# Optimization experiments

Hardware: AMD Instinct MI355X
Metric: run time of the kernel (lower is better)

The kernel has to match this reference:

```python
import jax, jax.numpy as jnp
import numpy as np

H = 16
D_MODEL = 1024
D_K = D_MODEL // H
WINDOW = 50
ROPE_BASE = 10000.0


def _rope_tables(seq_len, dim, dtype):
    inv_freq = 1.0 / (ROPE_BASE ** (jnp.arange(0, dim, 2, dtype=jnp.float32) / dim))
    t = jnp.arange(seq_len, dtype=jnp.float32)
    freqs = t[:, None] * inv_freq[None, :]          # [S, dim/2]
    emb = jnp.concatenate([freqs, freqs], axis=-1)  # [S, dim]
    return jnp.cos(emb).astype(dtype), jnp.sin(emb).astype(dtype)


def _rotate_half(x):
    d = x.shape[-1] // 2
    return jnp.concatenate([-x[..., d:], x[..., :d]], axis=-1)


def setup_inputs() -> dict:
    key = jax.random.key(0)
    ks = jax.random.split(key, 11)
    B, S = 2, 2048
    scale = 1.0 / np.sqrt(D_MODEL)
    inp = {
        'query': jax.random.normal(ks[0], (B, S, D_MODEL), jnp.float32),
        'key':   jax.random.normal(ks[1], (B, S, D_MODEL), jnp.float32),
        'value': jax.random.normal(ks[2], (B, S, D_MODEL), jnp.float32),
        'Wq': jax.random.normal(ks[3], (D_MODEL, D_MODEL), jnp.float32) * scale,
        'bq': jnp.zeros((D_MODEL,), jnp.float32),
        'Wk': jax.random.normal(ks[4], (D_MODEL, D_MODEL), jnp.float32) * scale,
        'bk': jnp.zeros((D_MODEL,), jnp.float32),
        'Wv': jax.random.normal(ks[5], (D_MODEL, D_MODEL), jnp.float32) * scale,
        'bv': jnp.zeros((D_MODEL,), jnp.float32),
        'Wo': jax.random.normal(ks[6], (D_MODEL, D_MODEL), jnp.float32) * scale,
        'bo': jnp.zeros((D_MODEL,), jnp.float32),
    }
    return inp


def reference(query, key, value, Wq, bq, Wk, bk, Wv, bv, Wo, bo):
    B, S, _ = query.shape
    # QKV projections (torch Linear: x @ W.T + b), split into heads -> [B,H,S,Dk]
    def proj(x, W, b):
        return (x @ W.T + b).reshape(B, S, H, D_K).transpose(0, 2, 1, 3)
    q = proj(query, Wq, bq)
    k = proj(key, Wk, bk)
    v = proj(value, Wv, bv)

    cos, sin = _rope_tables(S, D_K, q.dtype)  # [S, Dk]
    q = q * cos + _rotate_half(q) * sin
    k = k * cos + _rotate_half(k) * sin

    scores = jnp.einsum('bhqd,bhkd->bhqk', q, k) / np.sqrt(D_K)
    # sliding-window mask: |i-j| <= WINDOW
    idx = jnp.arange(S)
    dist = jnp.abs(idx[None, :] - idx[:, None])  # [S, S]
    scores = jnp.where(dist <= WINDOW, scores, jnp.asarray(-1e9, scores.dtype))

    p = jax.nn.softmax(scores, axis=-1)
    out = jnp.einsum('bhqk,bhkd->bhqd', p, v)          # [B,H,S,Dk]
    out = out.transpose(0, 2, 1, 3).reshape(B, S, D_MODEL)
    return out @ Wo.T + bo
```

## Files before the change

kernel.cpp:

```cpp
#include <hip/hip_runtime.h>
#include <hip/hip_bf16.h>
#include <math.h>

typedef __bf16 bf16_t;
typedef __bf16 bf16x8 __attribute__((ext_vector_type(8)));
typedef float floatx4 __attribute__((ext_vector_type(4)));
typedef unsigned int u32;

#define NHEAD 16

__device__ __forceinline__ void gload_lds16(const void* g, void* l) {
    __builtin_amdgcn_global_load_lds((const __attribute__((address_space(1))) u32*)g,
                                     (__attribute__((address_space(3))) u32*)l, 16, 0, 0);
}

__global__ __launch_bounds__(256) void k_prep(
    const float* __restrict__ q, const float* __restrict__ k, const float* __restrict__ v,
    const float* __restrict__ wq, const float* __restrict__ wk,
    const float* __restrict__ wv, const float* __restrict__ wo,
    bf16_t* __restrict__ Xq, bf16_t* __restrict__ Xk, bf16_t* __restrict__ Xv,
    bf16_t* __restrict__ Wqb, bf16_t* __restrict__ Wkb, bf16_t* __restrict__ Wvb,
    bf16_t* __restrict__ Wob, float* __restrict__ ct, float* __restrict__ st)
{
    int b = blockIdx.x;
    if (b < 8192) {
        const float* src; bf16_t* dst; int off;
        if      (b < 2048) { src = q;  dst = Xq;  off = b; }
        else if (b < 4096) { src = k;  dst = Xk;  off = b - 2048; }
        else if (b < 6144) { src = v;  dst = Xv;  off = b - 4096; }
        else if (b < 6656) { src = wq; dst = Wqb; off = b - 6144; }
        else if (b < 7168) { src = wk; dst = Wkb; off = b - 6656; }
        else if (b < 7680) { src = wv; dst = Wvb; off = b - 7168; }
        else               { src = wo; dst = Wob; off = b - 7680; }
        int i = (off * 256 + threadIdx.x) * 8;
        float4 a = *(const float4*)(src + i);
        float4 c = *(const float4*)(src + i + 4);
        bf16x8 o;
        o[0]=(bf16_t)a.x; o[1]=(bf16_t)a.y; o[2]=(bf16_t)a.z; o[3]=(bf16_t)a.w;
        o[4]=(bf16_t)c.x; o[5]=(bf16_t)c.y; o[6]=(bf16_t)c.z; o[7]=(bf16_t)c.w;
        *(bf16x8*)(dst + i) = o;
    } else {
        int idx = (b - 8192) * 256 + threadIdx.x;
        int s = idx >> 5, i = idx & 31;
        float e = (float)(2 * i) / 64.0f;
        float invf = 1.0f / powf(10000.0f, e);
        float ang = (float)s * invf;
        ct[idx] = cosf(ang);
        st[idx] = sinf(ang);
    }
}

__global__ __launch_bounds__(256,5) void k_gemm_qkv(
    const bf16_t* __restrict__ Xq, const bf16_t* __restrict__ Xk, const bf16_t* __restrict__ Xv,
    const bf16_t* __restrict__ Wqb, const bf16_t* __restrict__ Wkb, const bf16_t* __restrict__ Wvb,
    const float* __restrict__ bq, const float* __restrict__ bk, const float* __restrict__ bv,
    bf16_t* __restrict__ Qr, bf16_t* __restrict__ Kr, bf16_t* __restrict__ Vh,
    const float* __restrict__ ct, const float* __restrict__ st)
{
    __shared__ __align__(16) bf16_t As[2][4096];
    __shared__ __align__(16) bf16_t Bs[2][2048];

    int b0 = blockIdx.x;
    int wg = (b0 & 7) * 192 + (b0 >> 3);
    int id  = wg >> 9;
    int bid = wg & 511;
    int bmt = bid >> 4, bnt = bid & 15;

    const bf16_t* A   = (id==0) ? Xq  : (id==1) ? Xk  : Xv;
    const bf16_t* Wt  = (id==0) ? Wqb : (id==1) ? Wkb : Wvb;
    const float*  bias= (id==0) ? bq  : (id==1) ? bk  : bv;
    bf16_t* out = (id==0) ? Qr : (id==1) ? Kr : Vh;
    bool do_rope = (id < 2);

    int bm = bmt << 7;
    int bn = bnt << 6;
    int tid = threadIdx.x;
    int l = tid & 63, wid = tid >> 6;
    int fr = l & 15, kg = l >> 4;

    floatx4 acc[2][4];
    #pragma unroll
    for (int i = 0; i < 2; ++i)
        #pragma unroll
        for (int j = 0; j < 4; ++j) acc[i][j] = (floatx4){0.f,0.f,0.f,0.f};

    int srow = tid >> 2, scol = (tid & 3) << 3;
    const bf16_t* Ap0 = A  + ((size_t)(bm + srow) << 10) + scol;
    const bf16_t* Ap1 = A  + ((size_t)(bm + 64 + srow) << 10) + scol;
    const bf16_t* Bp  = Wt + ((size_t)(bn + srow) << 10) + scol;

    gload_lds16(Ap0, &As[0][tid << 3]);
    gload_lds16(Ap1, &As[0][(tid + 256) << 3]);
    gload_lds16(Bp,  &Bs[0][tid << 3]);
    __syncthreads();

    int cur = 0;
    for (int t = 0; t < 32; ++t) {
        if (t < 31) {
            int k0 = (t + 1) << 5;
            gload_lds16(Ap0 + k0, &As[cur ^ 1][tid << 3]);
            gload_lds16(Ap1 + k0, &As[cur ^ 1][(tid + 256) << 3]);
            gload_lds16(Bp  + k0, &Bs[cur ^ 1][tid << 3]);
        }
        bf16x8 af[2], bfr[4];
        #pragma unroll
        for (int i = 0; i < 2; ++i)
            af[i]  = *(const bf16x8*)&As[cur][((wid << 5) + (i << 4) + fr) * 32 + (kg << 3)];
        #pragma unroll
        for (int j = 0; j < 4; ++j)
            bfr[j] = *(const bf16x8*)&Bs[cur][((j << 4) + fr) * 32 + (kg << 3)];
        #pragma unroll
        for (int i = 0; i < 2; ++i)
            #pragma unroll
            for (int j = 0; j < 4; ++j)
                acc[i][j] = __builtin_amdgcn_mfma_f32_16x16x32_bf16(af[i], bfr[j], acc[i][j], 0, 0, 0);
        __syncthreads();
        cur ^= 1;
    }

    int h = bnt;
    #pragma unroll
    for (int i = 0; i < 2; ++i) {
        #pragma unroll
        for (int r = 0; r < 4; ++r) {
            int m  = bm + (wid << 5) + (i << 4) + (kg << 2) + r;
            int b_ = m >> 11, s_ = m & 2047;
            size_t ob = ((((size_t)(b_ * NHEAD + h)) << 11) + s_) << 6;
            if (do_rope) {
                #pragma unroll
                for (int j = 0; j < 2; ++j) {
                    int d = (j << 4) + fr;
                    float lo = acc[i][j][r]     + bias[bn + d];
                    float hv = acc[i][j + 2][r] + bias[bn + d + 32];
                    float c = ct[(s_ << 5) + d], sn = st[(s_ << 5) + d];
                    out[ob + d]      = (bf16_t)(lo * c - hv * sn);
                    out[ob + d + 32] = (bf16_t)(hv * c + lo * sn);
                }
            } else {
                #pragma unroll
                for (int j = 0; j < 4; ++j) {
                    int d = (j << 4) + fr;
                    out[ob + d] = (bf16_t)(acc[i][j][r] + bias[bn + d]);
                }
            }
        }
    }
}

__global__ __launch_bounds__(256,4) void k_gemm_o(
    const bf16_t* __restrict__ A, const bf16_t* __restrict__ Wt,
    const float* __restrict__ bias, float* __restrict__ out)
{
    __shared__ __align__(16) bf16_t As[2][2048];
    __shared__ __align__(16) bf16_t Bs[2][2048];

    int b0 = blockIdx.x;
    int wg = (b0 & 7) * 128 + (b0 >> 3);
    int bm = (wg >> 4) << 6;
    int bn = (wg & 15) << 6;
    int tid = threadIdx.x;
    int l = tid & 63, wid = tid >> 6;
    int fr = l & 15, kg = l >> 4;

    floatx4 acc[4];
    #pragma unroll
    for (int j = 0; j < 4; ++j) acc[j] = (floatx4){0.f,0.f,0.f,0.f};

    int srow = tid >> 2, scol = (tid & 3) << 3;
    const bf16_t* Ap = A  + ((size_t)(bm + srow) << 10) + scol;
    const bf16_t* Bp = Wt + ((size_t)(bn + srow) << 10) + scol;

    gload_lds16(Ap, &As[0][tid << 3]);
    gload_lds16(Bp, &Bs[0][tid << 3]);
    __syncthreads();

    int cur = 0;
    for (int t = 0; t < 32; ++t) {
        if (t < 31) {
            int k0 = (t + 1) << 5;
            gload_lds16(Ap + k0, &As[cur ^ 1][tid << 3]);
            gload_lds16(Bp + k0, &Bs[cur ^ 1][tid << 3]);
        }
        bf16x8 af, bfr[4];
        af = *(const bf16x8*)&As[cur][((wid << 4) + fr) * 32 + (kg << 3)];
        #pragma unroll
        for (int j = 0; j < 4; ++j)
            bfr[j] = *(const bf16x8*)&Bs[cur][((j << 4) + fr) * 32 + (kg << 3)];
        #pragma unroll
        for (int j = 0; j < 4; ++j)
            acc[j] = __builtin_amdgcn_mfma_f32_16x16x32_bf16(af, bfr[j], acc[j], 0, 0, 0);
        __syncthreads();
        cur ^= 1;
    }

    #pragma unroll
    for (int r = 0; r < 4; ++r) {
        int m = bm + (wid << 4) + (kg << 2) + r;
        #pragma unroll
        for (int j = 0; j < 4; ++j) {
            int n = bn + (j << 4) + fr;
            out[((size_t)m << 10) + n] = acc[j][r] + bias[n];
        }
    }
}

__global__ __launch_bounds__(256,2) void k_attn(
    const bf16_t* __restrict__ Qr, const bf16_t* __restrict__ Kr,
    const bf16_t* __restrict__ Vh, bf16_t* __restrict__ AO)
{
    __shared__ char smem[51200];
    bf16_t* KsPs = (bf16_t*)smem;
    bf16_t* Vt   = (bf16_t*)(smem + 25600);

    int q0 = blockIdx.x << 6;
    int h = blockIdx.y, b_ = blockIdx.z;
    int kstart = q0 - 64; if (kstart < 0) kstart = 0;
    int kend   = q0 + 128; if (kend > 2048) kend = 2048;
    int NR = kend - kstart;

    int tid = threadIdx.x, l = tid & 63, w = tid >> 6;
    int lane16 = l & 15, hi8 = (l >> 4) << 3;

    const bf16_t* Kbase = Kr + (((((size_t)(b_*NHEAD + h)) << 11) + kstart) << 6);
    const bf16_t* Vbase = Vh + (((((size_t)(b_*NHEAD + h)) << 11) + kstart) << 6);

    #pragma unroll
    for (int it = 0; it < 6; ++it) {
        int c = tid + (it << 8);
        int y = c << 4;
        int row = y >> 7, oz = y & 127;
        int srw = row < NR ? row : NR - 1;
        int src = (srw << 7) + (oz ^ ((row & 7) << 4));
        gload_lds16((const char*)Kbase + src, (char*)KsPs + y);
    }
    #pragma unroll
    for (int it = 0; it < 6; ++it) {
        int c = tid + (it << 8);
        int jd = c >> 3, d0 = (c & 7) << 3;
        int js = jd < NR ? jd : NR - 1;
        bf16x8 v8 = *(const bf16x8*)(Vbase + (js << 6) + d0);
        #pragma unroll
        for (int t = 0; t < 8; ++t) Vt[(d0 + t) * 200 + jd] = v8[t];
    }
    int qs = q0 + (w << 4) + lane16;
    const bf16_t* Qbase = Qr + (((((size_t)(b_*NHEAD + h)) << 11) + qs) << 6);
    bf16x8 qf0 = *(const bf16x8*)(Qbase + hi8);
    bf16x8 qf1 = *(const bf16x8*)(Qbase + 32 + hi8);

    __syncthreads();

    floatx4 sc[12];
    #pragma unroll
    for (int kt = 0; kt < 12; ++kt) {
        int row = (kt << 4) + lane16;
        int base = (row << 7) + (hi8 << 1);
        int swz = (row & 7) << 4;
        bf16x8 kf0 = *(const bf16x8*)((const char*)KsPs + (base ^ swz));
        bf16x8 kf1 = *(const bf16x8*)((const char*)KsPs + ((base + 64) ^ swz));
        floatx4 a = (floatx4){0.f,0.f,0.f,0.f};
        a = __builtin_amdgcn_mfma_f32_16x16x32_bf16(qf0, kf0, a, 0, 0, 0);
        a = __builtin_amdgcn_mfma_f32_16x16x32_bf16(qf1, kf1, a, 0, 0, 0);
        sc[kt] = a;
    }

    float inv_[4];
    #pragma unroll
    for (int r = 0; r < 4; ++r) {
        int qrow = q0 + (w << 4) + ((l >> 4) << 2) + r;
        float mx = -1e30f;
        #pragma unroll
        for (int kt = 0; kt < 12; ++kt) {
            int ks = kstart + (kt << 4) + lane16;
            int dd = qrow - ks; dd = dd < 0 ? -dd : dd;
            float sv = sc[kt][r] * 0.125f;
            sv = (dd <= 50 && ks < kend) ? sv : -1e30f;
            sc[kt][r] = sv;
            mx = fmaxf(mx, sv);
        }
        #pragma unroll
        for (int off = 1; off < 16; off <<= 1) mx = fmaxf(mx, __shfl_xor(mx, off));
        float sum = 0.f;
        #pragma unroll
        for (int kt = 0; kt < 12; ++kt) {
            float p = __expf(sc[kt][r] - mx);
            sc[kt][r] = p;
            sum += p;
        }
        #pragma unroll
        for (int off = 1; off < 16; off <<= 1) sum += __shfl_xor(sum, off);
        inv_[r] = 1.0f / sum;
    }

    __syncthreads();

    bf16_t* Pw = KsPs + w * 16 * 200;
    #pragma unroll
    for (int r = 0; r < 4; ++r) {
        int prow = ((l >> 4) << 2) + r;
        #pragma unroll
        for (int kt = 0; kt < 12; ++kt)
            Pw[prow * 200 + (kt << 4) + lane16] = (bf16_t)(sc[kt][r] * inv_[r]);
    }

    floatx4 oc[4];
    #pragma unroll
    for (int dt = 0; dt < 4; ++dt) oc[dt] = (floatx4){0.f,0.f,0.f,0.f};
    #pragma unroll
    for (int ks = 0; ks < 6; ++ks) {
        bf16x8 pf = *(const bf16x8*)&Pw[lane16 * 200 + (ks << 5) + hi8];
        #pragma unroll
        for (int dt = 0; dt < 4; ++dt) {
            bf16x8 vf = *(const bf16x8*)&Vt[((dt << 4) + lane16) * 200 + (ks << 5) + hi8];
            oc[dt] = __builtin_amdgcn_mfma_f32_16x16x32_bf16(pf, vf, oc[dt], 0, 0, 0);
        }
    }
    #pragma unroll
    for (int dt = 0; dt < 4; ++dt)
        #pragma unroll
        for (int r = 0; r < 4; ++r) {
            int qq = q0 + (w << 4) + ((l >> 4) << 2) + r;
            AO[(((size_t)(b_ * 2048 + qq)) << 10) + (h << 6) + (dt << 4) + lane16] = (bf16_t)oc[dt][r];
        }
}

extern "C" void kernel_launch(void* const* d_in, const int* in_sizes, int n_in,
                              void* d_out, int out_size, void* d_ws, size_t ws_size,
                              hipStream_t stream)
{
    const float* query = (const float*)d_in[0];
    const float* key_  = (const float*)d_in[1];
    const float* value = (const float*)d_in[2];
    const float* Wq = (const float*)d_in[3];
    const float* bq = (const float*)d_in[4];
    const float* Wk = (const float*)d_in[5];
    const float* bk = (const float*)d_in[6];
    const float* Wv = (const float*)d_in[7];
    const float* bv = (const float*)d_in[8];
    const float* Wo = (const float*)d_in[9];
    const float* bo = (const float*)d_in[10];

    char* ws = (char*)d_ws;
    bf16_t* Xq  = (bf16_t*)(ws);
    bf16_t* Xk  = (bf16_t*)(ws + 8388608);
    bf16_t* Xv  = (bf16_t*)(ws + 16777216);
    bf16_t* Wqb = (bf16_t*)(ws + 25165824);
    bf16_t* Wkb = (bf16_t*)(ws + 27262976);
    bf16_t* Wvb = (bf16_t*)(ws + 29360128);
    bf16_t* Wob = (bf16_t*)(ws + 31457280);
    bf16_t* Qr  = (bf16_t*)(ws + 33554432);
    bf16_t* Kr  = (bf16_t*)(ws + 41943040);
    bf16_t* Vh  = (bf16_t*)(ws + 50331648);
    bf16_t* AO  = (bf16_t*)(ws + 58720256);
    float*  ct  = (float*)(ws + 67108864);
    float*  st  = (float*)(ws + 67371008);

    k_prep<<<8448, 256, 0, stream>>>(query, key_, value, Wq, Wk, Wv, Wo,
                                     Xq, Xk, Xv, Wqb, Wkb, Wvb, Wob, ct, st);
    k_gemm_qkv<<<1536, 256, 0, stream>>>(Xq, Xk, Xv, Wqb, Wkb, Wvb,
                                         bq, bk, bv, Qr, Kr, Vh, ct, st);
    k_attn<<<dim3(32, 16, 2), 256, 0, stream>>>(Qr, Kr, Vh, AO);
    k_gemm_o<<<1024, 256, 0, stream>>>(AO, Wob, bo, (float*)d_out);
}
```

Baseline: 104.1 us.

## Enlarge QKV GEMM tiles to 128x128 and swizzle LDS layouts

The QKV projection GEMM moves from 128x64 to 128x128 block tiles on a 2x2 wave grid, halving the grid and raising operand reuse per LDS load. Both GEMMs reorder their global-to-LDS staging so each 16-row MFMA fragment sits in a contiguous 1KB chunk, aimed at avoiding LDS bank conflicts on fragment reads. The attention kernel adds XOR swizzles to the transposed V and P buffers for the same reason, and its occupancy hint rises from 2 to 3. The larger tile needs more accumulator registers and LDS per block, which lowers occupancy for the QKV GEMM.

```diff
diff --git a/kernel.cpp b/kernel.cpp
--- a/kernel.cpp
+++ b/kernel.cpp
@@ -50,7 +50,8 @@
     }
 }
 
-__global__ __launch_bounds__(256,5) void k_gemm_qkv(
+
+__global__ __launch_bounds__(256,3) void k_gemm_qkv(
     const bf16_t* __restrict__ Xq, const bf16_t* __restrict__ Xk, const bf16_t* __restrict__ Xv,
     const bf16_t* __restrict__ Wqb, const bf16_t* __restrict__ Wkb, const bf16_t* __restrict__ Wvb,
     const float* __restrict__ bq, const float* __restrict__ bk, const float* __restrict__ bv,
@@ -58,13 +59,12 @@
     const float* __restrict__ ct, const float* __restrict__ st)
 {
     __shared__ __align__(16) bf16_t As[2][4096];
-    __shared__ __align__(16) bf16_t Bs[2][2048];
+    __shared__ __align__(16) bf16_t Bs[2][4096];
 
     int b0 = blockIdx.x;
-    int wg = (b0 & 7) * 192 + (b0 >> 3);
-    int id  = wg >> 9;
-    int bid = wg & 511;
-    int bmt = bid >> 4, bnt = bid & 15;
+    int wg = (b0 & 7) * 96 + (b0 >> 3);
+    int id  = wg >> 8;
+    int bid = wg & 255;
 
     const bf16_t* A   = (id==0) ? Xq  : (id==1) ? Xk  : Xv;
     const bf16_t* Wt  = (id==0) ? Wqb : (id==1) ? Wkb : Wvb;
@@ -72,45 +72,50 @@
     bf16_t* out = (id==0) ? Qr : (id==1) ? Kr : Vh;
     bool do_rope = (id < 2);
 
-    int bm = bmt << 7;
-    int bn = bnt << 6;
+    int bm = (bid >> 3) << 7;
+    int bn = (bid & 7) << 7;
     int tid = threadIdx.x;
     int l = tid & 63, wid = tid >> 6;
+    int wr = wid >> 1, wc = wid & 1;
     int fr = l & 15, kg = l >> 4;
 
-    floatx4 acc[2][4];
-    #pragma unroll
-    for (int i = 0; i < 2; ++i)
+    floatx4 acc[4][4];
+    #pragma unroll
+    for (int i = 0; i < 4; ++i)
         #pragma unroll
         for (int j = 0; j < 4; ++j) acc[i][j] = (floatx4){0.f,0.f,0.f,0.f};
 
-    int srow = tid >> 2, scol = (tid & 3) << 3;
-    const bf16_t* Ap0 = A  + ((size_t)(bm + srow) << 10) + scol;
-    const bf16_t* Ap1 = A  + ((size_t)(bm + 64 + srow) << 10) + scol;
-    const bf16_t* Bp  = Wt + ((size_t)(bn + srow) << 10) + scol;
-
-    gload_lds16(Ap0, &As[0][tid << 3]);
-    gload_lds16(Ap1, &As[0][(tid + 256) << 3]);
-    gload_lds16(Bp,  &Bs[0][tid << 3]);
+    int c0 = tid, c1 = tid + 256;
+    int row0 = ((c0 >> 6) << 4) + (c0 & 15), sl0 = ((c0 >> 4) & 3) << 3;
+    int row1 = ((c1 >> 6) << 4) + (c1 & 15), sl1 = ((c1 >> 4) & 3) << 3;
+    const bf16_t* Ap0 = A  + ((size_t)(bm + row0) << 10) + sl0;
+    const bf16_t* Ap1 = A  + ((size_t)(bm + row1) << 10) + sl1;
+    const bf16_t* Bp0 = Wt + ((size_t)(bn + row0) << 10) + sl0;
+    const bf16_t* Bp1 = Wt + ((size_t)(bn + row1) << 10) + sl1;
+
+    gload_lds16(Ap0, &As[0][c0 << 3]);  gload_lds16(Ap1, &As[0][c1 << 3]);
+    gload_lds16(Bp0, &Bs[0][c0 << 3]);  gload_lds16(Bp1, &Bs[0][c1 << 3]);
     __syncthreads();
 
+    int a_off = (kg << 8) + (fr << 4);
     int cur = 0;
     for (int t = 0; t < 32; ++t) {
         if (t < 31) {
             int k0 = (t + 1) << 5;
-            gload_lds16(Ap0 + k0, &As[cur ^ 1][tid << 3]);
-            gload_lds16(Ap1 + k0, &As[cur ^ 1][(tid + 256) << 3]);
-            gload_lds16(Bp  + k0, &Bs[cur ^ 1][tid << 3]);
-        }
-        bf16x8 af[2], bfr[4];
-        #pragma unroll
-        for (int i = 0; i < 2; ++i)
-            af[i]  = *(const bf16x8*)&As[cur][((wid << 5) + (i << 4) + fr) * 32 + (kg << 3)];
+            gload_lds16(Ap0 + k0, &As[cur ^ 1][c0 << 3]);
+            gload_lds16(Ap1 + k0, &As[cur ^ 1][c1 << 3]);
+            gload_lds16(Bp0 + k0, &Bs[cur ^ 1][c0 << 3]);
+            gload_lds16(Bp1 + k0, &Bs[cur ^ 1][c1 << 3]);
+        }
+        bf16x8 af[4], bfr[4];
+        #pragma unroll
+        for (int i = 0; i < 4; ++i)
+            af[i]  = *(const bf16x8*)((const char*)As[cur] + (((wr << 2) + i) << 10) + a_off);
         #pragma unroll
         for (int j = 0; j < 4; ++j)
-            bfr[j] = *(const bf16x8*)&Bs[cur][((j << 4) + fr) * 32 + (kg << 3)];
-        #pragma unroll
-        for (int i = 0; i < 2; ++i)
+            bfr[j] = *(const bf16x8*)((const char*)Bs[cur] + (((wc << 2) + j) << 10) + a_off);
+        #pragma unroll
+        for (int i = 0; i < 4; ++i)
             #pragma unroll
             for (int j = 0; j < 4; ++j)
                 acc[i][j] = __builtin_amdgcn_mfma_f32_16x16x32_bf16(af[i], bfr[j], acc[i][j], 0, 0, 0);
@@ -118,29 +123,29 @@
         cur ^= 1;
     }
 
-    int h = bnt;
-    #pragma unroll
-    for (int i = 0; i < 2; ++i) {
+    int h = (bn + (wc<<6)) >> 6;
+    #pragma unroll
+    for (int i = 0; i < 4; ++i) {
         #pragma unroll
         for (int r = 0; r < 4; ++r) {
-            int m  = bm + (wid << 5) + (i << 4) + (kg << 2) + r;
+            int m  = bm + (wr<<6) + (i<<4) + (kg<<2) + r;
             int b_ = m >> 11, s_ = m & 2047;
-            size_t ob = ((((size_t)(b_ * NHEAD + h)) << 11) + s_) << 6;
+            size_t ob = ((((size_t)(b_*NHEAD + h)) << 11) + s_) << 6;
             if (do_rope) {
                 #pragma unroll
                 for (int j = 0; j < 2; ++j) {
-                    int d = (j << 4) + fr;
-                    float lo = acc[i][j][r]     + bias[bn + d];
-                    float hv = acc[i][j + 2][r] + bias[bn + d + 32];
-                    float c = ct[(s_ << 5) + d], sn = st[(s_ << 5) + d];
-                    out[ob + d]      = (bf16_t)(lo * c - hv * sn);
-                    out[ob + d + 32] = (bf16_t)(hv * c + lo * sn);
+                    int d = (j<<4) + fr;
+                    float lo = acc[i][j][r]   + bias[bn + (wc<<6) + d];
+                    float hv = acc[i][j+2][r] + bias[bn + (wc<<6) + d + 32];
+                    float c = ct[(s_<<5) + d], sn = st[(s_<<5) + d];
+                    out[ob + d]      = (bf16_t)(lo*c - hv*sn);
+                    out[ob + d + 32] = (bf16_t)(hv*c + lo*sn);
                 }
             } else {
                 #pragma unroll
                 for (int j = 0; j < 4; ++j) {
-                    int d = (j << 4) + fr;
-                    out[ob + d] = (bf16_t)(acc[i][j][r] + bias[bn + d]);
+                    int d = (j<<4) + fr;
+                    out[ob + d] = (bf16_t)(acc[i][j][r] + bias[bn + (wc<<6) + d]);
                 }
             }
         }
@@ -166,14 +171,15 @@
     #pragma unroll
     for (int j = 0; j < 4; ++j) acc[j] = (floatx4){0.f,0.f,0.f,0.f};
 
-    int srow = tid >> 2, scol = (tid & 3) << 3;
-    const bf16_t* Ap = A  + ((size_t)(bm + srow) << 10) + scol;
-    const bf16_t* Bp = Wt + ((size_t)(bn + srow) << 10) + scol;
+    int row0 = ((tid >> 6) << 4) + (tid & 15), sl0 = ((tid >> 4) & 3) << 3;
+    const bf16_t* Ap = A  + ((size_t)(bm + row0) << 10) + sl0;
+    const bf16_t* Bp = Wt + ((size_t)(bn + row0) << 10) + sl0;
 
     gload_lds16(Ap, &As[0][tid << 3]);
     gload_lds16(Bp, &Bs[0][tid << 3]);
     __syncthreads();
 
+    int a_off = (kg << 8) + (fr << 4);
     int cur = 0;
     for (int t = 0; t < 32; ++t) {
         if (t < 31) {
@@ -182,10 +188,10 @@
             gload_lds16(Bp + k0, &Bs[cur ^ 1][tid << 3]);
         }
         bf16x8 af, bfr[4];
-        af = *(const bf16x8*)&As[cur][((wid << 4) + fr) * 32 + (kg << 3)];
+        af = *(const bf16x8*)((const char*)As[cur] + (wid << 10) + a_off);
         #pragma unroll
         for (int j = 0; j < 4; ++j)
-            bfr[j] = *(const bf16x8*)&Bs[cur][((j << 4) + fr) * 32 + (kg << 3)];
+            bfr[j] = *(const bf16x8*)((const char*)Bs[cur] + (j << 10) + a_off);
         #pragma unroll
         for (int j = 0; j < 4; ++j)
             acc[j] = __builtin_amdgcn_mfma_f32_16x16x32_bf16(af, bfr[j], acc[j], 0, 0, 0);
@@ -204,13 +210,13 @@
     }
 }
 
-__global__ __launch_bounds__(256,2) void k_attn(
+__global__ __launch_bounds__(256,3) void k_attn(
     const bf16_t* __restrict__ Qr, const bf16_t* __restrict__ Kr,
     const bf16_t* __restrict__ Vh, bf16_t* __restrict__ AO)
 {
     __shared__ char smem[51200];
-    bf16_t* KsPs = (bf16_t*)smem;
-    bf16_t* Vt   = (bf16_t*)(smem + 25600);
+    char* KsPs = smem;
+    char* VtB  = smem + 25600;
 
     int q0 = blockIdx.x << 6;
     int h = blockIdx.y, b_ = blockIdx.z;
@@ -231,7 +237,7 @@
         int row = y >> 7, oz = y & 127;
         int srw = row < NR ? row : NR - 1;
         int src = (srw << 7) + (oz ^ ((row & 7) << 4));
-        gload_lds16((const char*)Kbase + src, (char*)KsPs + y);
+        gload_lds16((const char*)Kbase + src, KsPs + y);
     }
     #pragma unroll
     for (int it = 0; it < 6; ++it) {
@@ -240,7 +246,11 @@
         int js = jd < NR ? jd : NR - 1;
         bf16x8 v8 = *(const bf16x8*)(Vbase + (js << 6) + d0);
         #pragma unroll
-        for (int t = 0; t < 8; ++t) Vt[(d0 + t) * 200 + jd] = v8[t];
+        for (int t = 0; t < 8; ++t) {
+            int d = d0 + t;
+            int byte = d * 400 + (((jd << 1)) ^ (((d >> 3) & 7) << 4));
+            *(bf16_t*)(VtB + byte) = v8[t];
+        }
     }
     int qs = q0 + (w << 4) + lane16;
     const bf16_t* Qbase = Qr + (((((size_t)(b_*NHEAD + h)) << 11) + qs) << 6);
@@ -255,8 +265,8 @@
         int row = (kt << 4) + lane16;
         int base = (row << 7) + (hi8 << 1);
         int swz = (row & 7) << 4;
-        bf16x8 kf0 = *(const bf16x8*)((const char*)KsPs + (base ^ swz));
-        bf16x8 kf1 = *(const bf16x8*)((const char*)KsPs + ((base + 64) ^ swz));
+        bf16x8 kf0 = *(const bf16x8*)(KsPs + (base ^ swz));
+        bf16x8 kf1 = *(const bf16x8*)(KsPs + ((base + 64) ^ swz));
         floatx4 a = (floatx4){0.f,0.f,0.f,0.f};
         a = __builtin_amdgcn_mfma_f32_16x16x32_bf16(qf0, kf0, a, 0, 0, 0);
         a = __builtin_amdgcn_mfma_f32_16x16x32_bf16(qf1, kf1, a, 0, 0, 0);
@@ -293,24 +303,30 @@
 
     __syncthreads();
 
-    bf16_t* Pw = KsPs + w * 16 * 200;
+    char* PwB = KsPs + w * 6400;
     #pragma unroll
     for (int r = 0; r < 4; ++r) {
         int prow = ((l >> 4) << 2) + r;
-        #pragma unroll
-        for (int kt = 0; kt < 12; ++kt)
-            Pw[prow * 200 + (kt << 4) + lane16] = (bf16_t)(sc[kt][r] * inv_[r]);
+        int pm = ((prow >> 2) & 3) << 4;
+        #pragma unroll
+        for (int kt = 0; kt < 12; ++kt) {
+            int keyoff = ((kt << 4) + lane16) << 1;
+            *(bf16_t*)(PwB + prow * 400 + (keyoff ^ pm)) = (bf16_t)(sc[kt][r] * inv_[r]);
+        }
     }
 
     floatx4 oc[4];
     #pragma unroll
     for (int dt = 0; dt < 4; ++dt) oc[dt] = (floatx4){0.f,0.f,0.f,0.f};
+    int pm_r = ((lane16 >> 2) & 3) << 4;
     #pragma unroll
     for (int ks = 0; ks < 6; ++ks) {
-        bf16x8 pf = *(const bf16x8*)&Pw[lane16 * 200 + (ks << 5) + hi8];
+        int keyoff = ((ks << 5) + hi8) << 1;
+        bf16x8 pf = *(const bf16x8*)(PwB + lane16 * 400 + (keyoff ^ pm_r));
         #pragma unroll
         for (int dt = 0; dt < 4; ++dt) {
-            bf16x8 vf = *(const bf16x8*)&Vt[((dt << 4) + lane16) * 200 + (ks << 5) + hi8];
+            int d = (dt << 4) + lane16;
+            bf16x8 vf = *(const bf16x8*)(VtB + d * 400 + (keyoff ^ (((d >> 3) & 7) << 4)));
             oc[dt] = __builtin_amdgcn_mfma_f32_16x16x32_bf16(pf, vf, oc[dt], 0, 0, 0);
         }
     }
@@ -356,8 +372,8 @@
 
     k_prep<<<8448, 256, 0, stream>>>(query, key_, value, Wq, Wk, Wv, Wo,
                                      Xq, Xk, Xv, Wqb, Wkb, Wvb, Wob, ct, st);
-    k_gemm_qkv<<<1536, 256, 0, stream>>>(Xq, Xk, Xv, Wqb, Wkb, Wvb,
-                                         bq, bk, bv, Qr, Kr, Vh, ct, st);
+    k_gemm_qkv<<<768, 256, 0, stream>>>(Xq, Xk, Xv, Wqb, Wkb, Wvb,
+                                        bq, bk, bv, Qr, Kr, Vh, ct, st);
     k_attn<<<dim3(32, 16, 2), 256, 0, stream>>>(Qr, Kr, Vh, AO);
     k_gemm_o<<<1024, 256, 0, stream>>>(AO, Wob, bo, (float*)d_out);
 }
```

Measured after the change: 121.4 us. 16.6% more time.
